# Kernel optimization log

Measured on AMD Instinct MI355X. Metric: run time of the kernel, lower is better.

Reference implementation:

```python
import jax, jax.numpy as jnp
import numpy as np

EPS_NORM = 1e-12  # torch F.normalize eps
EPS_MM = 1e-08    # min-max denom eps


def setup_inputs() -> dict:
    key = jax.random.key(0)
    k1, k2 = jax.random.split(key)
    global_query = jax.random.normal(k1, (16, 256), dtype=jnp.float32)
    value = jax.random.normal(k2, (16, 256, 128, 128), dtype=jnp.float32)
    return {"global_query": global_query, "value": value}


def reference(global_query, value):
    # L2 normalize (torch.F.normalize: x / max(||x||, eps))
    q = global_query / jnp.maximum(
        jnp.linalg.norm(global_query, axis=-1, keepdims=True), EPS_NORM)
    v = value / jnp.maximum(
        jnp.linalg.norm(value, axis=1, keepdims=True), EPS_NORM)
    B, D, W, H = v.shape
    # score[b, w, h] = sum_d q[b,d] * v[b,d,w,h]  -> [B, W*H]
    score = jnp.einsum('bd,bdwh->bwh', q, v).reshape(B, W * H)
    # min/max computed under no_grad in the original -> stop_gradient
    max_s = jax.lax.stop_gradient(jnp.max(score, axis=1, keepdims=True))
    min_s = jax.lax.stop_gradient(jnp.min(score, axis=1, keepdims=True))
    attn = (score - min_s) / (max_s - min_s + EPS_MM)  # [B, W*H]
    attn = attn.reshape(B, 1, W, H)
    context = attn * v
    return (context, attn)
```

## Files before the change

### kernel.cpp

```cpp
#include <hip/hip_runtime.h>
#include <hip/hip_bf16.h>


#define B_  16
#define D_  256
#define WH_ 16384

__device__ __forceinline__ unsigned int fmap(float f) {
    unsigned int u = __float_as_uint(f);
    return (u & 0x80000000u) ? ~u : (u | 0x80000000u);
}
__device__ __forceinline__ float funmap(unsigned int u) {
    unsigned int b = (u & 0x80000000u) ? (u ^ 0x80000000u) : ~u;
    return __uint_as_float(b);
}

typedef float f32x4_t __attribute__((ext_vector_type(4)));
__device__ __forceinline__ void nt_store4(float* p, float4 v) {
    f32x4_t w = {v.x, v.y, v.z, v.w};
    __builtin_nontemporal_store(w, (f32x4_t*)p);
}

__global__ void init_mm_kernel(unsigned int* __restrict__ mm) {
    int i = threadIdx.x;
    if (i < 2 * B_) mm[i] = (i & 1) ? 0u : 0xFFFFFFFFu;
}

__global__ __launch_bounds__(256) void score_kernel(
    const float* __restrict__ q, const float* __restrict__ value,
    float* __restrict__ score, float* __restrict__ invn,
    unsigned int* __restrict__ mm)
{
    const int b   = blockIdx.y;
    const int tid = threadIdx.x;
    __shared__ float qs[D_];
    __shared__ float red[256];

    float qv = q[b * D_ + tid];
    red[tid] = qv * qv;
    __syncthreads();
    for (int s = 128; s > 0; s >>= 1) {
        if (tid < s) red[tid] += red[tid + s];
        __syncthreads();
    }
    float qnorm2 = red[0];
    __syncthreads();
    qs[tid] = qv * (1.0f / fmaxf(sqrtf(qnorm2), 1e-12f));
    __syncthreads();

    const int wh0 = (blockIdx.x * 256 + tid) * 4;
    const float* vb = value + (size_t)b * D_ * WH_ + wh0;
    float ss0 = 0.f, ss1 = 0.f, ss2 = 0.f, ss3 = 0.f;
    float dt0 = 0.f, dt1 = 0.f, dt2 = 0.f, dt3 = 0.f;
#pragma unroll 4
    for (int d = 0; d < D_; ++d) {
        float4 v4 = *(const float4*)(vb + (size_t)d * WH_);
        float qd = qs[d];
        ss0 += v4.x * v4.x; ss1 += v4.y * v4.y;
        ss2 += v4.z * v4.z; ss3 += v4.w * v4.w;
        dt0 += qd * v4.x;   dt1 += qd * v4.y;
        dt2 += qd * v4.z;   dt3 += qd * v4.w;
    }
    float n0 = 1.0f / fmaxf(sqrtf(ss0), 1e-12f);
    float n1 = 1.0f / fmaxf(sqrtf(ss1), 1e-12f);
    float n2 = 1.0f / fmaxf(sqrtf(ss2), 1e-12f);
    float n3 = 1.0f / fmaxf(sqrtf(ss3), 1e-12f);
    float s0 = dt0 * n0, s1 = dt1 * n1, s2 = dt2 * n2, s3 = dt3 * n3;

    *(float4*)(score + (size_t)b * WH_ + wh0) = make_float4(s0, s1, s2, s3);
    *(float4*)(invn  + (size_t)b * WH_ + wh0) = make_float4(n0, n1, n2, n3);

    float mn = fminf(fminf(s0, s1), fminf(s2, s3));
    float mx = fmaxf(fmaxf(s0, s1), fmaxf(s2, s3));
    red[tid] = mn;
    __syncthreads();
    for (int s = 128; s > 0; s >>= 1) {
        if (tid < s) red[tid] = fminf(red[tid], red[tid + s]);
        __syncthreads();
    }
    float bmn = red[0];
    __syncthreads();
    red[tid] = mx;
    __syncthreads();
    for (int s = 128; s > 0; s >>= 1) {
        if (tid < s) red[tid] = fmaxf(red[tid], red[tid + s]);
        __syncthreads();
    }
    if (tid == 0) {
        atomicMin(&mm[2 * b],     fmap(bmn));
        atomicMax(&mm[2 * b + 1], fmap(red[0]));
    }
}

__global__ __launch_bounds__(256) void ctx_kernel(
    const float* __restrict__ value, const float* __restrict__ score,
    const float* __restrict__ invn, const unsigned int* __restrict__ mm,
    float* __restrict__ out_ctx, float* __restrict__ out_attn)
{
    const int b   = blockIdx.y;
    const int wh0 = (blockIdx.x * 256 + threadIdx.x) * 4;

    const float mn = funmap(mm[2 * b]);
    const float sc = 1.0f / (funmap(mm[2 * b + 1]) - mn + 1e-8f);

    float4 s4 = *(const float4*)(score + (size_t)b * WH_ + wh0);
    float4 n4 = *(const float4*)(invn  + (size_t)b * WH_ + wh0);
    float4 a4;
    a4.x = (s4.x - mn) * sc; a4.y = (s4.y - mn) * sc;
    a4.z = (s4.z - mn) * sc; a4.w = (s4.w - mn) * sc;
    nt_store4(out_attn + (size_t)b * WH_ + wh0, a4);

    const float an0 = a4.x * n4.x, an1 = a4.y * n4.y;
    const float an2 = a4.z * n4.z, an3 = a4.w * n4.w;

    const float* vb = value   + (size_t)b * D_ * WH_ + wh0;
    float*       cb = out_ctx + (size_t)b * D_ * WH_ + wh0;
#pragma unroll 8
    for (int d = D_ - 1; d >= 0; --d) {
        float4 v4 = *(const float4*)(vb + (size_t)d * WH_);
        float4 c4;
        c4.x = an0 * v4.x; c4.y = an1 * v4.y;
        c4.z = an2 * v4.z; c4.w = an3 * v4.w;
        nt_store4(cb + (size_t)d * WH_, c4);
    }
}

extern "C" void kernel_launch(void* const* d_in, const int* in_sizes, int n_in,
                              void* d_out, int out_size, void* d_ws, size_t ws_size,
                              hipStream_t stream) {
    const float* q     = (const float*)d_in[0];
    const float* value = (const float*)d_in[1];

    float* out_ctx  = (float*)d_out;
    float* out_attn = out_ctx + (size_t)B_ * D_ * WH_;

    float* score = (float*)d_ws;
    float* invn  = score + (size_t)B_ * WH_;
    unsigned int* mm = (unsigned int*)(invn + (size_t)B_ * WH_);

    hipLaunchKernelGGL(init_mm_kernel, dim3(1), dim3(64), 0, stream, mm);
    hipLaunchKernelGGL(score_kernel, dim3(WH_ / 1024, B_), dim3(256), 0, stream,
                       q, value, score, invn, mm);
    hipLaunchKernelGGL(ctx_kernel, dim3(WH_ / 1024, B_), dim3(256),
                       0, stream, value, score, invn, mm, out_ctx, out_attn);
}
```

Baseline: 130.6 us.

## Split batch into two phases so value rereads hit Infinity Cache

Runs the score and context kernels in two phases of eight batches each, so the 128 MB slice of value read by the score pass can still be in the last-level cache when the context pass reads it again. Per-thread width is reduced from four to two elements to keep the block count per phase at 256. The cost is extra kernel launches and serialization between phases, plus narrower loads that may lower memory efficiency.

```diff
diff --git a/kernel.cpp b/kernel.cpp
--- a/kernel.cpp
+++ b/kernel.cpp
@@ -5,6 +5,7 @@
 #define B_  16
 #define D_  256
 #define WH_ 16384
+#define PHB 8
 
 __device__ __forceinline__ unsigned int fmap(float f) {
     unsigned int u = __float_as_uint(f);
@@ -15,10 +16,10 @@
     return __uint_as_float(b);
 }
 
-typedef float f32x4_t __attribute__((ext_vector_type(4)));
-__device__ __forceinline__ void nt_store4(float* p, float4 v) {
-    f32x4_t w = {v.x, v.y, v.z, v.w};
-    __builtin_nontemporal_store(w, (f32x4_t*)p);
+typedef float f32x2_t __attribute__((ext_vector_type(2)));
+__device__ __forceinline__ void nt_store2(float* p, float a, float b) {
+    f32x2_t w = {a, b};
+    __builtin_nontemporal_store(w, (f32x2_t*)p);
 }
 
 __global__ void init_mm_kernel(unsigned int* __restrict__ mm) {
@@ -29,9 +30,9 @@
 __global__ __launch_bounds__(256) void score_kernel(
     const float* __restrict__ q, const float* __restrict__ value,
     float* __restrict__ score, float* __restrict__ invn,
-    unsigned int* __restrict__ mm)
+    unsigned int* __restrict__ mm, int b_base)
 {
-    const int b   = blockIdx.y;
+    const int b   = b_base + blockIdx.y;
     const int tid = threadIdx.x;
     __shared__ float qs[D_];
     __shared__ float red[256];
@@ -48,30 +49,25 @@
     qs[tid] = qv * (1.0f / fmaxf(sqrtf(qnorm2), 1e-12f));
     __syncthreads();
 
-    const int wh0 = (blockIdx.x * 256 + tid) * 4;
+    const int wh0 = (blockIdx.x * 256 + tid) * 2;
     const float* vb = value + (size_t)b * D_ * WH_ + wh0;
-    float ss0 = 0.f, ss1 = 0.f, ss2 = 0.f, ss3 = 0.f;
-    float dt0 = 0.f, dt1 = 0.f, dt2 = 0.f, dt3 = 0.f;
-#pragma unroll 4
+    float ss0 = 0.f, ss1 = 0.f, dt0 = 0.f, dt1 = 0.f;
+#pragma unroll 16
     for (int d = 0; d < D_; ++d) {
-        float4 v4 = *(const float4*)(vb + (size_t)d * WH_);
+        float2 v2 = *(const float2*)(vb + (size_t)d * WH_);
         float qd = qs[d];
-        ss0 += v4.x * v4.x; ss1 += v4.y * v4.y;
-        ss2 += v4.z * v4.z; ss3 += v4.w * v4.w;
-        dt0 += qd * v4.x;   dt1 += qd * v4.y;
-        dt2 += qd * v4.z;   dt3 += qd * v4.w;
+        ss0 += v2.x * v2.x; ss1 += v2.y * v2.y;
+        dt0 += qd * v2.x;   dt1 += qd * v2.y;
     }
     float n0 = 1.0f / fmaxf(sqrtf(ss0), 1e-12f);
     float n1 = 1.0f / fmaxf(sqrtf(ss1), 1e-12f);
-    float n2 = 1.0f / fmaxf(sqrtf(ss2), 1e-12f);
-    float n3 = 1.0f / fmaxf(sqrtf(ss3), 1e-12f);
-    float s0 = dt0 * n0, s1 = dt1 * n1, s2 = dt2 * n2, s3 = dt3 * n3;
+    float s0 = dt0 * n0, s1 = dt1 * n1;
 
-    *(float4*)(score + (size_t)b * WH_ + wh0) = make_float4(s0, s1, s2, s3);
-    *(float4*)(invn  + (size_t)b * WH_ + wh0) = make_float4(n0, n1, n2, n3);
+    *(float2*)(score + (size_t)b * WH_ + wh0) = make_float2(s0, s1);
+    *(float2*)(invn  + (size_t)b * WH_ + wh0) = make_float2(n0, n1);
 
-    float mn = fminf(fminf(s0, s1), fminf(s2, s3));
-    float mx = fmaxf(fmaxf(s0, s1), fmaxf(s2, s3));
+    float mn = fminf(s0, s1);
+    float mx = fmaxf(s0, s1);
     red[tid] = mn;
     __syncthreads();
     for (int s = 128; s > 0; s >>= 1) {
@@ -95,33 +91,28 @@
 __global__ __launch_bounds__(256) void ctx_kernel(
     const float* __restrict__ value, const float* __restrict__ score,
     const float* __restrict__ invn, const unsigned int* __restrict__ mm,
-    float* __restrict__ out_ctx, float* __restrict__ out_attn)
+    float* __restrict__ out_ctx, float* __restrict__ out_attn, int b_base)
 {
-    const int b   = blockIdx.y;
-    const int wh0 = (blockIdx.x * 256 + threadIdx.x) * 4;
+    const int b   = b_base + blockIdx.y;
+    const int wh0 = (blockIdx.x * 256 + threadIdx.x) * 2;
 
     const float mn = funmap(mm[2 * b]);
     const float sc = 1.0f / (funmap(mm[2 * b + 1]) - mn + 1e-8f);
 
-    float4 s4 = *(const float4*)(score + (size_t)b * WH_ + wh0);
-    float4 n4 = *(const float4*)(invn  + (size_t)b * WH_ + wh0);
-    float4 a4;
-    a4.x = (s4.x - mn) * sc; a4.y = (s4.y - mn) * sc;
-    a4.z = (s4.z - mn) * sc; a4.w = (s4.w - mn) * sc;
-    nt_store4(out_attn + (size_t)b * WH_ + wh0, a4);
+    float2 s2 = *(const float2*)(score + (size_t)b * WH_ + wh0);
+    float2 n2 = *(const float2*)(invn  + (size_t)b * WH_ + wh0);
+    float a0 = (s2.x - mn) * sc;
+    float a1 = (s2.y - mn) * sc;
+    nt_store2(out_attn + (size_t)b * WH_ + wh0, a0, a1);
 
-    const float an0 = a4.x * n4.x, an1 = a4.y * n4.y;
-    const float an2 = a4.z * n4.z, an3 = a4.w * n4.w;
+    const float an0 = a0 * n2.x, an1 = a1 * n2.y;
 
     const float* vb = value   + (size_t)b * D_ * WH_ + wh0;
     float*       cb = out_ctx + (size_t)b * D_ * WH_ + wh0;
 #pragma unroll 8
     for (int d = D_ - 1; d >= 0; --d) {
-        float4 v4 = *(const float4*)(vb + (size_t)d * WH_);
-        float4 c4;
-        c4.x = an0 * v4.x; c4.y = an1 * v4.y;
-        c4.z = an2 * v4.z; c4.w = an3 * v4.w;
-        nt_store4(cb + (size_t)d * WH_, c4);
+        float2 v2 = *(const float2*)(vb + (size_t)d * WH_);
+        nt_store2(cb + (size_t)d * WH_, an0 * v2.x, an1 * v2.y);
     }
 }
 
@@ -139,8 +130,14 @@
     unsigned int* mm = (unsigned int*)(invn + (size_t)B_ * WH_);
 
     hipLaunchKernelGGL(init_mm_kernel, dim3(1), dim3(64), 0, stream, mm);
-    hipLaunchKernelGGL(score_kernel, dim3(WH_ / 1024, B_), dim3(256), 0, stream,
-                       q, value, score, invn, mm);
-    hipLaunchKernelGGL(ctx_kernel, dim3(WH_ / 1024, B_), dim3(256),
-                       0, stream, value, score, invn, mm, out_ctx, out_attn);
+
+    hipLaunchKernelGGL(score_kernel, dim3(32, PHB), dim3(256), 0, stream,
+                       q, value, score, invn, mm, 0);
+    hipLaunchKernelGGL(ctx_kernel, dim3(32, PHB), dim3(256), 0, stream,
+                       value, score, invn, mm, out_ctx, out_attn, 0);
+
+    hipLaunchKernelGGL(score_kernel, dim3(32, PHB), dim3(256), 0, stream,
+                       q, value, score, invn, mm, PHB);
+    hipLaunchKernelGGL(ctx_kernel, dim3(32, PHB), dim3(256), 0, stream,
+                       value, score, invn, mm, out_ctx, out_attn, PHB);
 }
```

New measurement: 150.6 us. +15.3%, slower.
